# Optimization experiments

Hardware: AMD Instinct MI355X
Metric: run time of the kernel (lower is better)

The kernel has to match this reference:

```python
import jax, jax.numpy as jnp
import numpy as np

B = 32          # patients
D = 128         # hidden dim (modality_embedding_dim == total_hidden_dim)
H = 4           # attention heads
DH = D // H     # per-head dim
L = 2           # num_graph_layers
N = {'ct': 1024, 'pet': 1024, 'clin': 256, 'gen': 2048, 'pat': 1}
# (src_type, dst_type) for the 8 relation types registered in _setup_relations
REL = [('ct','ct'), ('pet','pet'), ('clin','clin'), ('gen','gen'),
       ('pat','clin'), ('ct','gen'), ('pet','gen'), ('gen','pat')]
E_REL = [8192, 8192, 2048, 16384, 256, 8192, 8192, 2048]
EDGE_NAMES = ['e_ct','e_pet','e_clin','e_gen','e_pat2clin','e_ct2gen','e_pet2gen','e_gen2pat']


def setup_inputs() -> dict:
    key = jax.random.key(0)
    ks = iter(jax.random.split(key, 64))
    nk = lambda: next(ks)
    inp = {}
    inp['x_ct']   = jax.random.normal(nk(), (B, N['ct'],  D), jnp.float32)
    inp['x_pet']  = jax.random.normal(nk(), (B, N['pet'], D), jnp.float32)
    inp['x_clin'] = jax.random.normal(nk(), (B, N['clin'],D), jnp.float32)
    inp['x_gen']  = jax.random.normal(nk(), (B, N['gen'], D), jnp.float32)
    inp['early']  = jax.random.normal(nk(), (B, D), jnp.float32)

    def mk_edges(k, E, ns, nd):
        k1, k2 = jax.random.split(k)
        src = jax.random.randint(k1, (B, 1, E), 0, ns, jnp.int32)
        dst = jax.random.randint(k2, (B, 1, E), 0, nd, jnp.int32)
        return jnp.concatenate([src, dst], axis=1)  # [B,2,E]

    for nm, (s, d), E in zip(EDGE_NAMES, REL, E_REL):
        inp[nm] = mk_edges(nk(), E, N[s], N[d])

    sw = 1.0 / np.sqrt(D)
    inp['W_src'] = jax.random.normal(nk(), (L, 8, D, D), jnp.float32) * sw
    inp['W_dst'] = jax.random.normal(nk(), (L, 8, D, D), jnp.float32) * sw
    inp['a_src'] = jax.random.normal(nk(), (L, 8, H, DH), jnp.float32) * sw
    inp['a_dst'] = jax.random.normal(nk(), (L, 8, H, DH), jnp.float32) * sw
    inp['Wp'] = jax.random.normal(nk(), (3, D, D), jnp.float32) * sw  # CT, PET, genomic pooling
    inp['bp'] = jnp.zeros((3, D), jnp.float32)
    inp['W_sem'] = jax.random.normal(nk(), (4 * D, 128), jnp.float32) * (1.0 / np.sqrt(4 * D))
    inp['b_sem'] = jnp.zeros((128,), jnp.float32)
    inp['q_sem'] = jax.random.normal(nk(), (128,), jnp.float32) * sw
    return inp


def _leaky_relu(x):
    return jnp.where(x > 0, x, 0.2 * x)


def _gat_layer(x, edges, Ws, Wd, As, Ad):
    """One heterogeneous multi-head GAT layer summing over relation types."""
    agg = {t: jnp.zeros((B, N[t], H, DH), jnp.float32) for t in N}
    for r, ((s, d), ei) in enumerate(zip(REL, edges)):
        hs = jnp.einsum('bnd,de->bne', x[s], Ws[r]).reshape(B, N[s], H, DH)
        hd = jnp.einsum('bnd,de->bne', x[d], Wd[r]).reshape(B, N[d], H, DH)
        al_s = jnp.sum(hs * As[r], axis=-1)  # [B,Ns,H]
        al_d = jnp.sum(hd * Ad[r], axis=-1)  # [B,Nd,H]
        nd = N[d]

        def one(hs_b, as_b, ad_b, e_b):
            src, dst = e_b[0], e_b[1]
            logit = _leaky_relu(as_b[src] + ad_b[dst])                      # [E,H]
            m = jnp.full((nd, H), -1e30, logit.dtype).at[dst].max(logit)    # segment max
            p = jnp.exp(logit - m[dst])
            den = jnp.zeros((nd, H), p.dtype).at[dst].add(p)
            w = p / (den[dst] + 1e-16)                                      # edge softmax per dst node
            msg = w[:, :, None] * hs_b[src]                                 # [E,H,DH]
            return jnp.zeros((nd, H, DH), msg.dtype).at[dst].add(msg)

        agg[d] = agg[d] + jax.vmap(one)(hs, al_s, al_d, ei)
    return {t: jax.nn.elu(agg[t].reshape(B, N[t], D)) for t in N}


def _pool(feat, W, b):
    # query = Linear(mean(features)); scores = feat @ q; softmax-weighted sum
    q = jnp.mean(feat, axis=1) @ W + b            # [B,D]
    sc = jnp.einsum('bnd,bd->bn', feat, q)        # [B,N]
    w = jax.nn.softmax(sc, axis=1)
    return jnp.einsum('bn,bnd->bd', w, feat)      # [B,D]


def _forward(x_ct, x_pet, x_clin, x_gen, early, edges,
             W_src, W_dst, a_src, a_dst, Wp, bp, W_sem, b_sem, q_sem):
    x = {'ct': x_ct, 'pet': x_pet, 'clin': x_clin, 'gen': x_gen,
         'pat': early[:, None, :]}
    for l in range(L):
        x = _gat_layer(x, edges, W_src[l], W_dst[l], a_src[l], a_dst[l])
    ct_p  = _pool(x['ct'],  Wp[0], bp[0])
    pet_p = _pool(x['pet'], Wp[1], bp[1])
    gen_p = _pool(x['gen'], Wp[2], bp[2])   # shared across the 3 meta-paths
    pad = jnp.zeros((B, 2 * D), ct_p.dtype)  # pad 2D -> 4D as in original
    imm = jnp.concatenate([ct_p, gen_p, pad], axis=1)
    pro = jnp.concatenate([pet_p, gen_p, pad], axis=1)
    trt = jnp.concatenate([(ct_p + pet_p) * 0.5, gen_p, pad], axis=1)
    z = jnp.stack([imm, pro, trt], axis=1)                     # [B,3,4D]
    s = jnp.einsum('bpa,a->bp', jnp.tanh(jnp.einsum('bpf,fa->bpa', z, W_sem) + b_sem), q_sem)
    beta = jax.nn.softmax(s, axis=1)                           # [B,3]
    fused = jnp.einsum('bp,bpf->bf', beta, z)                  # [B,4D]
    return fused, beta


def reference(x_ct, x_pet, x_clin, x_gen, early,
              e_ct, e_pet, e_clin, e_gen, e_pat2clin, e_ct2gen, e_pet2gen, e_gen2pat,
              W_src, W_dst, a_src, a_dst, Wp, bp, W_sem, b_sem, q_sem):
    edges = [e_ct, e_pet, e_clin, e_gen, e_pat2clin, e_ct2gen, e_pet2gen, e_gen2pat]
    return _forward(x_ct, x_pet, x_clin, x_gen, early, edges,
                    W_src, W_dst, a_src, a_dst, Wp, bp, W_sem, b_sem, q_sem)
```

## Files before the change

### kernel.cpp

```cpp
#include <hip/hip_runtime.h>
#include <math.h>

static constexpr int NB = 32;
static constexpr int ND = 128;

typedef short bf16x8 __attribute__((ext_vector_type(8)));
typedef float f32x4  __attribute__((ext_vector_type(4)));
typedef unsigned short u16x8 __attribute__((ext_vector_type(8)));

__device__ __forceinline__ float lrelu(float x){ return x > 0.f ? x : 0.2f*x; }
__device__ __forceinline__ unsigned short f2b(float f){
  unsigned u = __float_as_uint(f);
  return (unsigned short)((u + 0x7FFFu + ((u>>16)&1u)) >> 16);
}
__device__ __forceinline__ float b2f(unsigned short b){
  return __uint_as_float(((unsigned)b) << 16);
}

__global__ __launch_bounds__(128) void k_fold(const float* __restrict__ Wsrc,
    const float* __restrict__ Wdst, const float* __restrict__ asrc,
    const float* __restrict__ adst, float* __restrict__ vbuf){
  const int wid[5] = {0,1,3,5,6};
  int lr = blockIdx.x, role = blockIdx.y, l = blockIdx.z;
  int r = wid[lr];
  const float* W = (role ? Wdst : Wsrc) + (size_t)(l*8+r)*16384;
  const float* a = (role ? adst : asrc) + (size_t)(l*8+r)*128;
  int k = threadIdx.x;
  float* o = vbuf + ((size_t)((l*5+lr)*2+role))*512 + k*4;
  #pragma unroll
  for(int h=0;h<4;h++){
    float s = 0.f;
    #pragma unroll
    for(int j=0;j<32;j++) s += W[k*128 + h*32 + j]*a[h*32 + j];
    o[h] = s;
  }
}

__global__ __launch_bounds__(256) void k_wpack(const float* __restrict__ Wsrc,
    unsigned short* __restrict__ Wf){
  const int wid[5] = {0,1,3,5,6};
  int lr = blockIdx.x, l = blockIdx.y;
  const float* W = Wsrc + (size_t)(l*8+wid[lr])*16384;
  unsigned short* o = Wf + (size_t)((l*5+lr)*4)*4096;
  for(int idx=threadIdx.x; idx<128*128; idx+=256){
    int k = idx >> 7, col = idx & 127;
    int h = col >> 5, cc = col & 31;
    int k4 = k>>2, g = k4&3, kk = k4>>3, j = 4*((k4>>2)&1) + (k&3);
    int nb = cc>>4, lane = (cc&15) + 16*g;
    o[(size_t)h*4096 + ((size_t)((kk*2+nb)*64 + lane))*8 + j] = f2b(W[k*128 + col]);
  }
}

struct CsrP {
  const int* eg[5];
  int l2E[5];
  int Nd_[5];
  int roff_[5];
  int eoff_[5];
};

__global__ __launch_bounds__(512) void k_csr(CsrP P, int* __restrict__ rowstart,
                                             int* __restrict__ srcidx){
  int b = blockIdx.x, r = blockIdx.y, t = threadIdx.x;
  int E = 1<<P.l2E[r], Nd = P.Nd_[r];
  const int* eg = P.eg[r] + (size_t)b*2*E;
  int* rsO = rowstart + P.roff_[r] + b*(Nd+1);
  int* siO = srcidx + P.eoff_[r] + (size_t)b*E;
  __shared__ int cnt[2048];
  __shared__ int wsums[8];
  for(int i=t;i<Nd;i+=512) cnt[i]=0;
  __syncthreads();
  for(int e=t;e<E;e+=512) atomicAdd(&cnt[eg[E+e]], 1);
  __syncthreads();
  int C = Nd >> 9;
  int base = t*C;
  int loc[4]; int s_=0;
  for(int i=0;i<C;i++){ loc[i]=cnt[base+i]; s_+=loc[i]; }
  int lane = t&63, wv = t>>6;
  int sinc = s_;
  #pragma unroll
  for(int off=1;off<64;off<<=1){
    int u = __shfl_up(sinc, off);
    if(lane>=off) sinc += u;
  }
  if(lane==63) wsums[wv]=sinc;
  __syncthreads();
  int wbase=0, total=0;
  #pragma unroll
  for(int i=0;i<8;i++){ int v=wsums[i]; if(i<wv) wbase+=v; total+=v; }
  int excl = wbase + sinc - s_;
  for(int i=0;i<C;i++){
    int idx=base+i;
    rsO[idx]=excl; cnt[idx]=excl; excl+=loc[i];
  }
  if(t==0) rsO[Nd]=total;
  __syncthreads();
  for(int e=t;e<E;e+=512){
    int src=eg[e], dst=eg[E+e];
    int pos=atomicAdd(&cnt[dst],1);
    siO[pos]=src;
  }
}

struct HsP {
  int tb[4];
  int usef;
  const float* xf[3];
  unsigned long long xoff[3];
  int Ns[3];
  int nW[3];
  unsigned long long wfo[3][2];
  unsigned long long hso[3][2];
  unsigned long long aso[3][2];
  unsigned long long asrco[3][2];
  int nvd[3];
  unsigned long long vdo[3][3];
  unsigned long long aldo2[3][3];
  int ndd[3][3];
};

__global__ __launch_bounds__(256) void k_hs(HsP P, const unsigned short* __restrict__ x16,
    const unsigned short* __restrict__ Wf, const float* __restrict__ asrc,
    const float* __restrict__ vbuf, unsigned short* __restrict__ hs,
    float* __restrict__ als, float* __restrict__ ald){
  __shared__ unsigned short xl[16*132];
  int B = blockIdx.x;
  int t=0; while(t<2 && B>=P.tb[t+1]) t++;
  int local = B - P.tb[t];
  int b = local & 31, tile = local >> 5;
  int n0 = tile*16;
  int tid = threadIdx.x, w = tid>>6, ln = tid&63;
  if(P.usef){
    const float* xf = P.xf[t] + ((size_t)((size_t)b*P.Ns[t] + n0))*128;
    int row = tid>>4, c8 = tid&15;
    float4 a = *(const float4*)(xf + (size_t)row*128 + c8*8);
    float4 c = *(const float4*)(xf + (size_t)row*128 + c8*8 + 4);
    u16x8 r;
    r[0]=f2b(a.x); r[1]=f2b(a.y); r[2]=f2b(a.z); r[3]=f2b(a.w);
    r[4]=f2b(c.x); r[5]=f2b(c.y); r[6]=f2b(c.z); r[7]=f2b(c.w);
    *(u16x8*)&xl[row*132 + c8*8] = r;
  } else {
    int row = tid>>4, ch = tid&15;
    u16x8 v = *(const u16x8*)(x16 + P.xoff[t] + ((size_t)((size_t)b*P.Ns[t] + n0+row)*128 + ch*8));
    *(u16x8*)&xl[row*132 + ch*8] = v;
  }
  __syncthreads();
  int g = ln>>4, r15 = ln&15;
  for(int rep=0; rep<P.nW[t]; rep++){
    const unsigned short* wf = Wf + P.wfo[t][rep] + (size_t)w*4096;
    f32x4 acc[2]; acc[0]=(f32x4){0,0,0,0}; acc[1]=(f32x4){0,0,0,0};
    #pragma unroll
    for(int kk=0;kk<4;kk++){
      const unsigned short* pa = &xl[r15*132 + kk*32 + 4*g];
      ushort4 lo = *(const ushort4*)pa;
      ushort4 hi = *(const ushort4*)(pa+16);
      union { ushort u[8]; bf16x8 v; } tmp;
      tmp.u[0]=lo.x; tmp.u[1]=lo.y; tmp.u[2]=lo.z; tmp.u[3]=lo.w;
      tmp.u[4]=hi.x; tmp.u[5]=hi.y; tmp.u[6]=hi.z; tmp.u[7]=hi.w;
      bf16x8 af = tmp.v;
      #pragma unroll
      for(int nb=0;nb<2;nb++){
        bf16x8 bw = *(const bf16x8*)(wf + ((size_t)((kk*2+nb)*64 + ln))*8);
        acc[nb] = __builtin_amdgcn_mfma_f32_16x16x32_bf16(af, bw, acc[nb], 0, 0, 0);
      }
    }
    unsigned short* ho = hs + P.hso[t][rep] + ((size_t)b*P.Ns[t] + n0)*128;
    #pragma unroll
    for(int qq=0;qq<4;qq++){
      int m = 4*g + qq;
      #pragma unroll
      for(int nb=0;nb<2;nb++){
        ho[(size_t)m*128 + w*32 + nb*16 + r15] = f2b(acc[nb][qq]);
      }
    }
    {
      const float* aS = asrc + P.asrco[t][rep];
      float a0v = aS[w*32 + r15], a1v = aS[w*32 + 16 + r15];
      float p0 = acc[0][0]*a0v + acc[1][0]*a1v;
      float p1 = acc[0][1]*a0v + acc[1][1]*a1v;
      float p2 = acc[0][2]*a0v + acc[1][2]*a1v;
      float p3 = acc[0][3]*a0v + acc[1][3]*a1v;
      #pragma unroll
      for(int off=1; off<16; off<<=1){
        p0 += __shfl_xor(p0,off); p1 += __shfl_xor(p1,off);
        p2 += __shfl_xor(p2,off); p3 += __shfl_xor(p3,off);
      }
      if(r15 < 4){
        float pv = (r15==0)?p0:((r15==1)?p1:((r15==2)?p2:p3));
        als[P.aso[t][rep] + ((size_t)b*P.Ns[t] + n0 + 4*g + r15)*4 + w] = pv;
      }
    }
  }
  int nvd = P.nvd[t];
  if(tid < (nvd<<6)){
    int vd = tid>>6, rem = tid&63, row = rem>>2, h = rem&3;
    const float* vv = vbuf + P.vdo[t][vd];
    float s = 0.f;
    #pragma unroll 8
    for(int k=0;k<128;k++) s += b2f(xl[row*132+k]) * vv[k*4+h];
    ald[P.aldo2[t][vd] + ((size_t)b*P.ndd[t][vd] + n0 + row)*4 + h] = s;
  }
}

static constexpr int WSL = 240;

struct Fu5P {
  int nrel[3], ndshift[3];
  int roff[3][3], eoff[3][3], E[3][3], Ns[3][3];
  int rowbase[3][3];
  unsigned long long aldo[3][3];
  unsigned long long outoff[3];
};

__global__ __launch_bounds__(512, 8) void k_fuse7(Fu5P P,
    const int* __restrict__ rowstart, const int* __restrict__ srcidx,
    const float* __restrict__ als, const float* __restrict__ ald,
    const unsigned short* __restrict__ hs, unsigned short* __restrict__ out16){
  __shared__ float wlds_all[8*4*WSL];
  __shared__ int   silds_all[8*WSL];
  int B = blockIdx.x;
  int w = threadIdx.x >> 6, ln = threadIdx.x & 63;
  int xcd = B & 7, slot = B >> 3;
  int bg = slot >> 6, rem = slot & 63;
  int b = bg*8 + xcd;
  int v = rem*8 + w;
  int g = v >> 2, k4 = v & 3;
  int t, tile;
  if(k4 < 2){ t = 0; tile = g*2 + k4; }
  else if(k4 == 2){ t = 1; tile = g; }
  else { t = 2; tile = g; }
  int Nd = 1 << P.ndshift[t];
  int d0 = tile * 8;
  int nrel = P.nrel[t];
  float* wlds = wlds_all + w*4*WSL;
  int*  silds = silds_all + w*WSL;
  int dst = ln >> 3, sub = ln & 7;
  int d = d0 + dst;

  int len0=0, len1=0, len2=0, s00=0, s01=0, s02=0;
  {
    const int* rsq = rowstart + P.roff[t][0] + b*(Nd+1);
    s00 = rsq[d]; len0 = rsq[d+1] - s00;
  }
  if(nrel > 1){
    const int* rsq1 = rowstart + P.roff[t][1] + b*(Nd+1);
    s01 = rsq1[d]; len1 = rsq1[d+1] - s01;
    const int* rsq2 = rowstart + P.roff[t][2] + b*(Nd+1);
    s02 = rsq2[d]; len2 = rsq2[d+1] - s02;
  }
  int clen = len0 + len1 + len2;
  int mybase = 0;
  #pragma unroll
  for(int dd=0; dd<7; dd++){
    int vl = __shfl(clen, dd*8);
    if(dd < dst) mybase += vl;
  }

  auto dorel = [&](int q, int s0q, int lq, int segb){
    const int* si = srcidx + P.eoff[t][q] + (size_t)b*P.E[t][q] + s0q;
    int bake = P.rowbase[t][q] + b*P.Ns[t][q];
    float4 ad4 = *(const float4*)(ald + P.aldo[t][q] + ((size_t)b*Nd + d)*4);
    float dn0=0.f, dn1=0.f, dn2=0.f, dn3=0.f;
    for(int i=sub; i<lq; i+=8){
      int e = segb + i;
      int sil = bake + si[i];
      silds[e] = sil;
      float4 as4 = *(const float4*)(als + 4*(size_t)sil);
      float p0 = __expf(lrelu(as4.x+ad4.x));
      float p1 = __expf(lrelu(as4.y+ad4.y));
      float p2 = __expf(lrelu(as4.z+ad4.z));
      float p3 = __expf(lrelu(as4.w+ad4.w));
      wlds[0*WSL+e]=p0; wlds[1*WSL+e]=p1; wlds[2*WSL+e]=p2; wlds[3*WSL+e]=p3;
      dn0+=p0; dn1+=p1; dn2+=p2; dn3+=p3;
    }
    dn0+=__shfl_xor(dn0,1); dn1+=__shfl_xor(dn1,1); dn2+=__shfl_xor(dn2,1); dn3+=__shfl_xor(dn3,1);
    dn0+=__shfl_xor(dn0,2); dn1+=__shfl_xor(dn1,2); dn2+=__shfl_xor(dn2,2); dn3+=__shfl_xor(dn3,2);
    dn0+=__shfl_xor(dn0,4); dn1+=__shfl_xor(dn1,4); dn2+=__shfl_xor(dn2,4); dn3+=__shfl_xor(dn3,4);
    float i0=1.f/(dn0+1e-16f), i1=1.f/(dn1+1e-16f);
    float i2=1.f/(dn2+1e-16f), i3=1.f/(dn3+1e-16f);
    for(int i=sub; i<lq; i+=8){
      int e = segb + i;
      wlds[0*WSL+e]*=i0; wlds[1*WSL+e]*=i1;
      wlds[2*WSL+e]*=i2; wlds[3*WSL+e]*=i3;
    }
  };
  dorel(0, s00, len0, mybase);
  if(nrel > 1){
    dorel(1, s01, len1, mybase + len0);
    dorel(2, s02, len2, mybase + len0 + len1);
  }
  __builtin_amdgcn_wave_barrier();

  int h = ln>>4;
  int run = 0;
  #pragma unroll
  for(int it=0; it<8; it++){
    int cl = __shfl(clen, it*8);
    int e0 = run, e1 = run + cl; run = e1;
    float a0 = 0.f, a1 = 0.f;
    int e = e0;
    int eal = (e0+3)&~3; if(eal > e1) eal = e1;
    for(; e<eal; e++){
      float wv = wlds[h*WSL + e];
      unsigned vv = *(const unsigned*)(hs + ((size_t)silds[e]*128 + 2*ln));
      a0 += wv*__uint_as_float(vv<<16);
      a1 += wv*__uint_as_float(vv&0xFFFF0000u);
    }
    for(; e+8<=e1; e+=8){
      int4  sq0 = *(const int4*)&silds[e];
      int4  sq1 = *(const int4*)&silds[e+4];
      float4 wq0 = *(const float4*)&wlds[h*WSL + e];
      float4 wq1 = *(const float4*)&wlds[h*WSL + e + 4];
      unsigned v0 = *(const unsigned*)(hs + ((size_t)sq0.x*128 + 2*ln));
      unsigned v1 = *(const unsigned*)(hs + ((size_t)sq0.y*128 + 2*ln));
      unsigned v2 = *(const unsigned*)(hs + ((size_t)sq0.z*128 + 2*ln));
      unsigned v3 = *(const unsigned*)(hs + ((size_t)sq0.w*128 + 2*ln));
      unsigned v4 = *(const unsigned*)(hs + ((size_t)sq1.x*128 + 2*ln));
      unsigned v5 = *(const unsigned*)(hs + ((size_t)sq1.y*128 + 2*ln));
      unsigned v6 = *(const unsigned*)(hs + ((size_t)sq1.z*128 + 2*ln));
      unsigned v7 = *(const unsigned*)(hs + ((size_t)sq1.w*128 + 2*ln));
      a0 += wq0.x*__uint_as_float(v0<<16); a1 += wq0.x*__uint_as_float(v0&0xFFFF0000u);
      a0 += wq0.y*__uint_as_float(v1<<16); a1 += wq0.y*__uint_as_float(v1&0xFFFF0000u);
      a0 += wq0.z*__uint_as_float(v2<<16); a1 += wq0.z*__uint_as_float(v2&0xFFFF0000u);
      a0 += wq0.w*__uint_as_float(v3<<16); a1 += wq0.w*__uint_as_float(v3&0xFFFF0000u);
      a0 += wq1.x*__uint_as_float(v4<<16); a1 += wq1.x*__uint_as_float(v4&0xFFFF0000u);
      a0 += wq1.y*__uint_as_float(v5<<16); a1 += wq1.y*__uint_as_float(v5&0xFFFF0000u);
      a0 += wq1.z*__uint_as_float(v6<<16); a1 += wq1.z*__uint_as_float(v6&0xFFFF0000u);
      a0 += wq1.w*__uint_as_float(v7<<16); a1 += wq1.w*__uint_as_float(v7&0xFFFF0000u);
    }
    for(; e+4<=e1; e+=4){
      int4  sq = *(const int4*)&silds[e];
      float4 wq = *(const float4*)&wlds[h*WSL + e];
      unsigned v0 = *(const unsigned*)(hs + ((size_t)sq.x*128 + 2*ln));
      unsigned v1 = *(const unsigned*)(hs + ((size_t)sq.y*128 + 2*ln));
      unsigned v2 = *(const unsigned*)(hs + ((size_t)sq.z*128 + 2*ln));
      unsigned v3 = *(const unsigned*)(hs + ((size_t)sq.w*128 + 2*ln));
      a0 += wq.x*__uint_as_float(v0<<16); a1 += wq.x*__uint_as_float(v0&0xFFFF0000u);
      a0 += wq.y*__uint_as_float(v1<<16); a1 += wq.y*__uint_as_float(v1&0xFFFF0000u);
      a0 += wq.z*__uint_as_float(v2<<16); a1 += wq.z*__uint_as_float(v2&0xFFFF0000u);
      a0 += wq.w*__uint_as_float(v3<<16); a1 += wq.w*__uint_as_float(v3&0xFFFF0000u);
    }
    for(; e<e1; e++){
      float wv = wlds[h*WSL + e];
      unsigned vv = *(const unsigned*)(hs + ((size_t)silds[e]*128 + 2*ln));
      a0 += wv*__uint_as_float(vv<<16);
      a1 += wv*__uint_as_float(vv&0xFFFF0000u);
    }
    int m = d0 + it;
    float o0 = a0 > 0.f ? a0 : expm1f(a0);
    float o1 = a1 > 0.f ? a1 : expm1f(a1);
    ushort2 o; o.x = f2b(o0); o.y = f2b(o1);
    *(ushort2*)(out16 + P.outoff[t] + ((size_t)b*Nd + m)*128 + 2*ln) = o;
  }
}

__device__ __constant__ const size_t POFF[3] = {0ull, 4194304ull, 8388608ull};
__device__ __constant__ const int    PNN[3]  = {1024, 1024, 2048};
static constexpr int PCH = 64;
static constexpr int MAXCH = 32;

__global__ __launch_bounds__(128) void k_pool_psum(const unsigned short* __restrict__ x2,
    float* __restrict__ part){
  int p = blockIdx.z, b = blockIdx.x, c = blockIdx.y, t = threadIdx.x;
  int Nn = PNN[p];
  if(c*PCH >= Nn) return;
  const unsigned short* f = x2 + POFF[p] + ((size_t)b*Nn + c*PCH)*ND;
  float acc = 0.f;
  #pragma unroll 8
  for(int n=0;n<PCH;n++) acc += b2f(f[(size_t)n*ND + t]);
  part[(((size_t)p*NB + b)*MAXCH + c)*ND + t] = acc;
}

__global__ __launch_bounds__(128) void k_pool_q(const float* __restrict__ part,
    const float* __restrict__ Wp, const float* __restrict__ bp,
    float* __restrict__ q){
  int p = blockIdx.z, b = blockIdx.x, t = threadIdx.x;
  int nch = PNN[p]/PCH;
  __shared__ float mean[ND];
  float s = 0.f;
  for(int c=0;c<nch;c++) s += part[(((size_t)p*NB + b)*MAXCH + c)*ND + t];
  mean[t] = s / (float)PNN[p];
  __syncthreads();
  const float* W = Wp + (size_t)p*ND*ND;
  float qv = bp[p*ND + t];
  #pragma unroll 8
  for(int k=0;k<ND;k++) qv += mean[k]*W[k*ND + t];
  q[((size_t)p*NB + b)*ND + t] = qv;
}

__global__ __launch_bounds__(256) void k_pool_score(const unsigned short* __restrict__ x2,
    const float* __restrict__ q, float* __restrict__ sc){
  int p = blockIdx.z, b = blockIdx.y;
  int w = threadIdx.x >> 6, lane = threadIdx.x & 63;
  int n = blockIdx.x*4 + w;
  int Nn = PNN[p];
  if(n >= Nn) return;
  const unsigned short* f  = x2 + POFF[p] + ((size_t)b*Nn + n)*ND;
  const float* qb = q + ((size_t)p*NB + b)*ND;
  float s = b2f(f[lane])*qb[lane] + b2f(f[lane+64])*qb[lane+64];
  #pragma unroll
  for(int off=32; off; off>>=1) s += __shfl_xor(s, off);
  if(lane == 0) sc[((size_t)p*NB + b)*2048 + n] = s;
}

__global__ __launch_bounds__(256) void k_pool_smax(const float* __restrict__ sc,
    float* __restrict__ stat){
  int p = blockIdx.z, b = blockIdx.x, t = threadIdx.x;
  int Nn = PNN[p];
  __shared__ float red[256];
  const float* s = sc + ((size_t)p*NB + b)*2048;
  float mx = -1e30f;
  for(int n=t;n<Nn;n+=256) mx = fmaxf(mx, s[n]);
  red[t] = mx; __syncthreads();
  for(int o=128;o;o>>=1){ if(t<o) red[t]=fmaxf(red[t],red[t+o]); __syncthreads(); }
  mx = red[0]; __syncthreads();
  float sum = 0.f;
  for(int n=t;n<Nn;n+=256) sum += __expf(s[n]-mx);
  red[t] = sum; __syncthreads();
  for(int o=128;o;o>>=1){ if(t<o) red[t]+=red[t+o]; __syncthreads(); }
  if(t==0){ stat[((size_t)p*NB + b)*2] = mx; stat[((size_t)p*NB + b)*2+1] = 1.f/red[0]; }
}

__global__ __launch_bounds__(128) void k_pool_wsum(const unsigned short* __restrict__ x2,
    const float* __restrict__ sc, const float* __restrict__ stat,
    float* __restrict__ part){
  int p = blockIdx.z, b = blockIdx.x, c = blockIdx.y, t = threadIdx.x;
  int Nn = PNN[p];
  if(c*PCH >= Nn) return;
  __shared__ float wsh[PCH];
  float mx  = stat[((size_t)p*NB + b)*2];
  float inv = stat[((size_t)p*NB + b)*2+1];
  if(t < PCH) wsh[t] = __expf(sc[((size_t)p*NB + b)*2048 + c*PCH + t] - mx)*inv;
  __syncthreads();
  const unsigned short* f = x2 + POFF[p] + ((size_t)b*Nn + c*PCH)*ND;
  float acc = 0.f;
  #pragma unroll 8
  for(int n=0;n<PCH;n++) acc += wsh[n]*b2f(f[(size_t)n*ND + t]);
  part[(((size_t)p*NB + b)*MAXCH + c)*ND + t] = acc;
}

__global__ __launch_bounds__(128) void k_pool_comb(const float* __restrict__ part,
    float* __restrict__ pooled){
  int p = blockIdx.z, b = blockIdx.x, t = threadIdx.x;
  int nch = PNN[p]/PCH;
  float s = 0.f;
  for(int c=0;c<nch;c++) s += part[(((size_t)p*NB + b)*MAXCH + c)*ND + t];
  pooled[((size_t)p*NB + b)*ND + t] = s;
}

__global__ __launch_bounds__(128) void k_sem(const float* __restrict__ ctp,
    const float* __restrict__ petp, const float* __restrict__ genp,
    const float* __restrict__ Wsem, const float* __restrict__ bsem,
    const float* __restrict__ qsem, float* __restrict__ fused, float* __restrict__ beta){
  int b = blockIdx.x, t = threadIdx.x;
  __shared__ float z[3][256];
  __shared__ float red[128];
  float ct = ctp[b*ND + t], pet = petp[b*ND + t], gen = genp[b*ND + t];
  z[0][t]=ct;  z[1][t]=pet; z[2][t]=0.5f*(ct+pet);
  z[0][ND+t]=gen; z[1][ND+t]=gen; z[2][ND+t]=gen;
  __syncthreads();
  float s[3];
  for(int p=0;p<3;p++){
    float a = bsem[t];
    for(int f=0;f<256;f++) a += z[p][f]*Wsem[f*128 + t];
    a = tanhf(a);
    red[t] = a * qsem[t];
    __syncthreads();
    for(int o=64;o>0;o>>=1){ if(t<o) red[t]+=red[t+o]; __syncthreads(); }
    s[p] = red[0]; __syncthreads();
  }
  float mx = fmaxf(s[0], fmaxf(s[1], s[2]));
  float e0 = __expf(s[0]-mx), e1 = __expf(s[1]-mx), e2 = __expf(s[2]-mx);
  float sm = e0+e1+e2;
  float b0 = e0/sm, b1 = e1/sm, b2 = e2/sm;
  if(t < 3) beta[b*3 + t] = (t==0)?b0:((t==1)?b1:b2);
  float f0 = b0*z[0][t] + b1*z[1][t] + b2*z[2][t];
  float f1 = b0*z[0][ND+t] + b1*z[1][ND+t] + b2*z[2][ND+t];
  fused[(size_t)b*512 + t]       = f0;
  fused[(size_t)b*512 + 128 + t] = f1;
  fused[(size_t)b*512 + 256 + t] = 0.f;
  fused[(size_t)b*512 + 384 + t] = 0.f;
}

extern "C" void kernel_launch(void* const* d_in, const int* in_sizes, int n_in,
                              void* d_out, int out_size, void* d_ws, size_t ws_size,
                              hipStream_t stream) {
  static const int wid[5]    = {0,1,3,5,6};
  static const int edgein[5] = {5,6,8,10,11};
  static const int l2E[5]    = {13,13,14,13,13};
  static const int Nd_l[5]   = {1024,1024,2048,2048,2048};
  static const int E_l[5]    = {8192,8192,16384,8192,8192};
  static const int Ns_l[5]   = {1024,1024,2048,1024,1024};
  static const int eoff[6]   = {0,262144,524288,1048576,1310720,1572864};
  static const int roff[5]   = {0,32800,65600,131168,196736};
  static const unsigned long long aoff[5]   = {0,131072,262144,524288,655360};
  static const unsigned long long aldoff[5] = {0,131072,262144,524288,786432};
  static const unsigned long long hsoff_lr[5] = {0ull,4194304ull,8388608ull,16777216ull,20971520ull};
  static const unsigned long long ALD = 786432;

  const float* Wsrc = (const float*)d_in[13];
  const float* Wp   = (const float*)d_in[17];
  const float* bp   = (const float*)d_in[18];
  const float* Wsem = (const float*)d_in[19];
  const float* bsem = (const float*)d_in[20];
  const float* qsem = (const float*)d_in[21];

  unsigned short* xc16 = (unsigned short*)d_ws;
  unsigned short* x2b16 = xc16;
  unsigned short* xmid16 = xc16 + 16777216;
  float* albase = (float*)(xmid16 + 16777216);
  float* als = albase;
  float* ald = albase + ALD;
  float* vbuf = albase + 1835008;
  unsigned short* wfbuf = (unsigned short*)(vbuf + 10240);
  float* pooled = (float*)(wfbuf + 163840);
  float* part = pooled + 12288;
  float* qbuf = part + 393216;
  float* scbuf = qbuf + 12288;
  float* stat = scbuf + 196608;
  int* rowstart = (int*)(stat + 192);
  int* srcidx = rowstart + 262304;
  unsigned short* hs16 = (unsigned short*)(srcidx + 1572864);

  { dim3 g(5,2,2); k_fold<<<g,128,0,stream>>>(Wsrc, (const float*)d_in[14],
                                              (const float*)d_in[15], (const float*)d_in[16], vbuf); }
  { dim3 g(5,2); k_wpack<<<g,256,0,stream>>>(Wsrc, wfbuf); }

  CsrP csr;
  for(int r=0;r<5;r++){
    csr.eg[r] = (const int*)d_in[edgein[r]];
    csr.l2E[r] = l2E[r]; csr.Nd_[r] = Nd_l[r];
    csr.roff_[r] = roff[r]; csr.eoff_[r] = eoff[r];
  }
  { dim3 g(NB,5); k_csr<<<g,512,0,stream>>>(csr, rowstart, srcidx); }

  static const unsigned long long xoo[3] = {0,4194304,8388608};
  static const int t2_nrel[3] = {3,1,1};
  static const int t2_lrel[3][3] = {{2,3,4},{0,0,0},{1,0,0}};
  static const int t2_nds[3] = {11,10,10};
  static const int t2_out[3] = {2,0,1};

  Fu5P fp;
  for(int t=0;t<3;t++){
    fp.nrel[t]=t2_nrel[t]; fp.ndshift[t]=t2_nds[t]; fp.outoff[t]=xoo[t2_out[t]];
    for(int q=0;q<3;q++){
      int lr = t2_lrel[t][q];
      fp.roff[t][q]=roff[lr]; fp.eoff[t][q]=eoff[lr];
      fp.E[t][q]=E_l[lr]; fp.Ns[t][q]=Ns_l[lr];
      fp.rowbase[t][q]=(int)(aoff[lr]/4);
      fp.aldo[t][q]=aldoff[lr];
    }
  }

  static const int hs_lr[3][2] = {{0,3},{1,4},{2,2}};
  static const int vd_lr[3][3] = {{0,0,0},{1,0,0},{2,3,4}};
  HsP hp;
  hp.tb[0]=0; hp.tb[1]=2048; hp.tb[2]=4096; hp.tb[3]=8192;
  hp.xf[0]=(const float*)d_in[0]; hp.xf[1]=(const float*)d_in[1]; hp.xf[2]=(const float*)d_in[3];
  hp.xoff[0]=0; hp.xoff[1]=4194304; hp.xoff[2]=8388608;
  hp.Ns[0]=1024; hp.Ns[1]=1024; hp.Ns[2]=2048;
  hp.nW[0]=2; hp.nW[1]=2; hp.nW[2]=1;
  hp.nvd[0]=1; hp.nvd[1]=1; hp.nvd[2]=3;
  for(int t=0;t<3;t++){
    for(int rep=0;rep<2;rep++){
      int lr = hs_lr[t][rep];
      hp.hso[t][rep]=hsoff_lr[lr];
      hp.aso[t][rep]=aoff[lr];
    }
    for(int vd=0;vd<3;vd++){
      int lr = vd_lr[t][vd];
      hp.aldo2[t][vd]=aldoff[lr];
      hp.ndd[t][vd]=Nd_l[lr];
    }
  }
  hp.hso[2][1]=0; hp.aso[2][1]=0;

  for(int l=0;l<2;l++){
    unsigned short* xout = (l==0) ? xmid16 : x2b16;
    hp.usef = (l==0) ? 1 : 0;

    for(int t=0;t<3;t++){
      for(int rep=0;rep<2;rep++){
        int lr = hs_lr[t][rep];
        hp.wfo[t][rep]=(unsigned long long)((l*5 + lr)*4)*4096;
        hp.asrco[t][rep]=(unsigned long long)((l*8 + wid[lr])*128);
      }
      for(int vd=0;vd<3;vd++){
        int lr = vd_lr[t][vd];
        hp.vdo[t][vd]=((unsigned long long)((l*5+lr)*2+1))*512;
      }
    }
    k_hs<<<8192,256,0,stream>>>(hp, xmid16, wfbuf, (const float*)d_in[15], vbuf,
                                hs16, als, ald);

    k_fuse7<<<2048,512,0,stream>>>(fp, rowstart, srcidx, als, ald, hs16, xout);
  }

  {
    dim3 gchunk(NB, MAXCH, 3);
    dim3 gone(NB, 1, 3);
    dim3 gscore(512, NB, 3);
    k_pool_psum <<<gchunk,128,0,stream>>>(x2b16, part);
    k_pool_q    <<<gone,  128,0,stream>>>(part, Wp, bp, qbuf);
    k_pool_score<<<gscore,256,0,stream>>>(x2b16, qbuf, scbuf);
    k_pool_smax <<<gone,  256,0,stream>>>(scbuf, stat);
    k_pool_wsum <<<gchunk,128,0,stream>>>(x2b16, scbuf, stat, part);
    k_pool_comb <<<gone,  128,0,stream>>>(part, pooled);
  }

  float* fused = (float*)d_out;
  float* beta  = fused + (size_t)NB*512;
  k_sem<<<NB,128,0,stream>>>(pooled, pooled + NB*ND, pooled + 2*NB*ND,
                             Wsem, bsem, qsem, fused, beta);
}
```

Before: 323.3 us.

## Double k_hs row tile, reuse register weights, stage outputs through LDS

The k_hs projection kernel now handles 32 rows per block instead of 16, halving the grid. Weight fragments are loaded into registers once per rep and reused across both 16-row MFMA chunks. The bf16 outputs are staged in an LDS buffer and written back as coalesced 16-byte vector stores instead of scattered 2-byte stores. This adds LDS use, extra barriers and register pressure, and halves the number of blocks available for occupancy.

```diff
diff --git a/kernel.cpp b/kernel.cpp
--- a/kernel.cpp
+++ b/kernel.cpp
@@ -123,59 +123,69 @@
     const unsigned short* __restrict__ Wf, const float* __restrict__ asrc,
     const float* __restrict__ vbuf, unsigned short* __restrict__ hs,
     float* __restrict__ als, float* __restrict__ ald){
-  __shared__ unsigned short xl[16*132];
+  __shared__ unsigned short xl[32*132];
+  __shared__ unsigned short obuf[32*136];
   int B = blockIdx.x;
   int t=0; while(t<2 && B>=P.tb[t+1]) t++;
   int local = B - P.tb[t];
   int b = local & 31, tile = local >> 5;
-  int n0 = tile*16;
+  int n0 = tile*32;
   int tid = threadIdx.x, w = tid>>6, ln = tid&63;
-  if(P.usef){
-    const float* xf = P.xf[t] + ((size_t)((size_t)b*P.Ns[t] + n0))*128;
-    int row = tid>>4, c8 = tid&15;
-    float4 a = *(const float4*)(xf + (size_t)row*128 + c8*8);
-    float4 c = *(const float4*)(xf + (size_t)row*128 + c8*8 + 4);
-    u16x8 r;
-    r[0]=f2b(a.x); r[1]=f2b(a.y); r[2]=f2b(a.z); r[3]=f2b(a.w);
-    r[4]=f2b(c.x); r[5]=f2b(c.y); r[6]=f2b(c.z); r[7]=f2b(c.w);
-    *(u16x8*)&xl[row*132 + c8*8] = r;
-  } else {
-    int row = tid>>4, ch = tid&15;
-    u16x8 v = *(const u16x8*)(x16 + P.xoff[t] + ((size_t)((size_t)b*P.Ns[t] + n0+row)*128 + ch*8));
-    *(u16x8*)&xl[row*132 + ch*8] = v;
+  {
+    int row = tid>>3, c16 = (tid&7)*16;
+    if(P.usef){
+      const float* xf = P.xf[t] + ((size_t)((size_t)b*P.Ns[t] + n0 + row))*128 + c16;
+      #pragma unroll
+      for(int half=0; half<2; half++){
+        float4 a = *(const float4*)(xf + half*8);
+        float4 c = *(const float4*)(xf + half*8 + 4);
+        u16x8 r;
+        r[0]=f2b(a.x); r[1]=f2b(a.y); r[2]=f2b(a.z); r[3]=f2b(a.w);
+        r[4]=f2b(c.x); r[5]=f2b(c.y); r[6]=f2b(c.z); r[7]=f2b(c.w);
+        *(u16x8*)&xl[row*132 + c16 + half*8] = r;
+      }
+    } else {
+      const unsigned short* xb = x16 + P.xoff[t] + ((size_t)((size_t)b*P.Ns[t] + n0 + row))*128 + c16;
+      u16x8 v0 = *(const u16x8*)xb;
+      u16x8 v1 = *(const u16x8*)(xb + 8);
+      *(u16x8*)&xl[row*132 + c16]     = v0;
+      *(u16x8*)&xl[row*132 + c16 + 8] = v1;
+    }
   }
   __syncthreads();
   int g = ln>>4, r15 = ln&15;
   for(int rep=0; rep<P.nW[t]; rep++){
     const unsigned short* wf = Wf + P.wfo[t][rep] + (size_t)w*4096;
-    f32x4 acc[2]; acc[0]=(f32x4){0,0,0,0}; acc[1]=(f32x4){0,0,0,0};
+    bf16x8 bw[8];
     #pragma unroll
     for(int kk=0;kk<4;kk++){
-      const unsigned short* pa = &xl[r15*132 + kk*32 + 4*g];
-      ushort4 lo = *(const ushort4*)pa;
-      ushort4 hi = *(const ushort4*)(pa+16);
-      union { ushort u[8]; bf16x8 v; } tmp;
-      tmp.u[0]=lo.x; tmp.u[1]=lo.y; tmp.u[2]=lo.z; tmp.u[3]=lo.w;
-      tmp.u[4]=hi.x; tmp.u[5]=hi.y; tmp.u[6]=hi.z; tmp.u[7]=hi.w;
-      bf16x8 af = tmp.v;
       #pragma unroll
-      for(int nb=0;nb<2;nb++){
-        bf16x8 bw = *(const bf16x8*)(wf + ((size_t)((kk*2+nb)*64 + ln))*8);
-        acc[nb] = __builtin_amdgcn_mfma_f32_16x16x32_bf16(af, bw, acc[nb], 0, 0, 0);
+      for(int nb=0;nb<2;nb++)
+        bw[kk*2+nb] = *(const bf16x8*)(wf + ((size_t)((kk*2+nb)*64 + ln))*8);
+    }
+    const float* aS = asrc + P.asrco[t][rep];
+    float a0v = aS[w*32 + r15], a1v = aS[w*32 + 16 + r15];
+    #pragma unroll
+    for(int c=0;c<2;c++){
+      f32x4 acc[2]; acc[0]=(f32x4){0,0,0,0}; acc[1]=(f32x4){0,0,0,0};
+      #pragma unroll
+      for(int kk=0;kk<4;kk++){
+        const unsigned short* pa = &xl[(c*16 + r15)*132 + kk*32 + 4*g];
+        ushort4 lo = *(const ushort4*)pa;
+        ushort4 hi = *(const ushort4*)(pa+16);
+        union { ushort u[8]; bf16x8 v; } tmp;
+        tmp.u[0]=lo.x; tmp.u[1]=lo.y; tmp.u[2]=lo.z; tmp.u[3]=lo.w;
+        tmp.u[4]=hi.x; tmp.u[5]=hi.y; tmp.u[6]=hi.z; tmp.u[7]=hi.w;
+        bf16x8 af = tmp.v;
+        acc[0] = __builtin_amdgcn_mfma_f32_16x16x32_bf16(af, bw[kk*2+0], acc[0], 0, 0, 0);
+        acc[1] = __builtin_amdgcn_mfma_f32_16x16x32_bf16(af, bw[kk*2+1], acc[1], 0, 0, 0);
       }
-    }
-    unsigned short* ho = hs + P.hso[t][rep] + ((size_t)b*P.Ns[t] + n0)*128;
-    #pragma unroll
-    for(int qq=0;qq<4;qq++){
-      int m = 4*g + qq;
       #pragma unroll
-      for(int nb=0;nb<2;nb++){
-        ho[(size_t)m*128 + w*32 + nb*16 + r15] = f2b(acc[nb][qq]);
+      for(int qq=0;qq<4;qq++){
+        int m = c*16 + 4*g + qq;
+        obuf[m*136 + w*32 + r15]      = f2b(acc[0][qq]);
+        obuf[m*136 + w*32 + 16 + r15] = f2b(acc[1][qq]);
       }
-    }
-    {
-      const float* aS = asrc + P.asrco[t][rep];
-      float a0v = aS[w*32 + r15], a1v = aS[w*32 + 16 + r15];
       float p0 = acc[0][0]*a0v + acc[1][0]*a1v;
       float p1 = acc[0][1]*a0v + acc[1][1]*a1v;
       float p2 = acc[0][2]*a0v + acc[1][2]*a1v;
@@ -187,18 +197,28 @@
       }
       if(r15 < 4){
         float pv = (r15==0)?p0:((r15==1)?p1:((r15==2)?p2:p3));
-        als[P.aso[t][rep] + ((size_t)b*P.Ns[t] + n0 + 4*g + r15)*4 + w] = pv;
+        als[P.aso[t][rep] + ((size_t)b*P.Ns[t] + n0 + c*16 + 4*g + r15)*4 + w] = pv;
       }
     }
+    __syncthreads();
+    {
+      unsigned short* ho = hs + P.hso[t][rep] + ((size_t)b*P.Ns[t] + n0)*128;
+      int row = tid>>3, c16 = (tid&7)*16;
+      u16x8 o0 = *(const u16x8*)&obuf[row*136 + c16];
+      u16x8 o1 = *(const u16x8*)&obuf[row*136 + c16 + 8];
+      *(u16x8*)(ho + (size_t)row*128 + c16)     = o0;
+      *(u16x8*)(ho + (size_t)row*128 + c16 + 8) = o1;
+    }
+    __syncthreads();
   }
   int nvd = P.nvd[t];
-  if(tid < (nvd<<6)){
-    int vd = tid>>6, rem = tid&63, row = rem>>2, h = rem&3;
+  for(int s=tid; s<(nvd<<7); s+=256){
+    int vd = s>>7, rem = s&127, row = rem>>2, h = rem&3;
     const float* vv = vbuf + P.vdo[t][vd];
-    float s = 0.f;
+    float sum = 0.f;
     #pragma unroll 8
-    for(int k=0;k<128;k++) s += b2f(xl[row*132+k]) * vv[k*4+h];
-    ald[P.aldo2[t][vd] + ((size_t)b*P.ndd[t][vd] + n0 + row)*4 + h] = s;
+    for(int k=0;k<128;k++) sum += b2f(xl[row*132+k]) * vv[k*4+h];
+    ald[P.aldo2[t][vd] + ((size_t)b*P.ndd[t][vd] + n0 + row)*4 + h] = sum;
   }
 }
 
@@ -555,7 +575,7 @@
   static const int hs_lr[3][2] = {{0,3},{1,4},{2,2}};
   static const int vd_lr[3][3] = {{0,0,0},{1,0,0},{2,3,4}};
   HsP hp;
-  hp.tb[0]=0; hp.tb[1]=2048; hp.tb[2]=4096; hp.tb[3]=8192;
+  hp.tb[0]=0; hp.tb[1]=1024; hp.tb[2]=2048; hp.tb[3]=4096;
   hp.xf[0]=(const float*)d_in[0]; hp.xf[1]=(const float*)d_in[1]; hp.xf[2]=(const float*)d_in[3];
   hp.xoff[0]=0; hp.xoff[1]=4194304; hp.xoff[2]=8388608;
   hp.Ns[0]=1024; hp.Ns[1]=1024; hp.Ns[2]=2048;
@@ -590,7 +610,7 @@
         hp.vdo[t][vd]=((unsigned long long)((l*5+lr)*2+1))*512;
       }
     }
-    k_hs<<<8192,256,0,stream>>>(hp, xmid16, wfbuf, (const float*)d_in[15], vbuf,
+    k_hs<<<4096,256,0,stream>>>(hp, xmid16, wfbuf, (const float*)d_in[15], vbuf,
                                 hs16, als, ald);
 
     k_fuse7<<<2048,512,0,stream>>>(fp, rowstart, srcidx, als, ald, hs16, xout);
```

New measurement: 325.8 us, median of 2. No clear change (+0.8%).
